# Optimization experiments

Measured on AMD Instinct MI355X. Metric: run time of the kernel, lower is better.

Reference implementation:

```python
import jax, jax.numpy as jnp
from jax import lax
import numpy as np

B, W, M, F = 8, 20, 512, 16
H = 128          # n_hidden
HALF = 64        # half_hid
K = 10           # conv out channels
LONG_K = W // 2  # dilated conv kernel


def setup_inputs() -> dict:
    key = jax.random.key(0)
    ks = jax.random.split(key, 24)
    s = 0.1  # weight scale (xavier-ish)
    return {
        "X": jax.random.normal(ks[0], (B, W, M, F), jnp.float32),
        "Y": jax.random.uniform(ks[1], (B, M), jnp.float32),
        "adj": jax.random.uniform(ks[2], (M, M), jnp.float32),
        "V": jax.random.normal(ks[3], (HALF,), jnp.float32) * s,
        "bv": jax.random.normal(ks[4], (1,), jnp.float32) * s,
        "W1": jax.random.normal(ks[5], (HALF, H), jnp.float32) * s,
        "b1": jax.random.normal(ks[6], (HALF,), jnp.float32) * s,
        "W2": jax.random.normal(ks[7], (HALF, H), jnp.float32) * s,
        "Wb": jax.random.normal(ks[8], (M, M), jnp.float32) * s,
        "wb": jax.random.normal(ks[9], (1,), jnp.float32) * s,
        "conv_w": jax.random.normal(ks[10], (K, F, W), jnp.float32) * s,
        "conv_b": jax.random.normal(ks[11], (K,), jnp.float32) * s,
        "convl_w": jax.random.normal(ks[12], (K, F, LONG_K), jnp.float32) * s,
        "convl_b": jax.random.normal(ks[13], (K,), jnp.float32) * s,
        "gru_Wih": jax.random.normal(ks[14], (3 * H, F), jnp.float32) * s,
        "gru_Whh": jax.random.normal(ks[15], (3 * H, H), jnp.float32) * s,
        "gru_bih": jax.random.normal(ks[16], (3 * H,), jnp.float32) * s,
        "gru_bhh": jax.random.normal(ks[17], (3 * H,), jnp.float32) * s,
        "gc1_W": jax.random.normal(ks[18], (3 * K, H), jnp.float32) * s,
        "gc1_b": jax.random.normal(ks[19], (H,), jnp.float32) * s,
        "gc2_W": jax.random.normal(ks[20], (H, K), jnp.float32) * s,
        "gc2_b": jax.random.normal(ks[21], (K,), jnp.float32) * s,
        "out_W": jax.random.normal(ks[22], (1, H + K), jnp.float32) * s,
        "out_b": jax.random.normal(ks[23], (1,), jnp.float32) * s,
    }


def _gru_last(xseq, Wih, Whh, bih, bhh):
    # xseq: (N, T, F) -> last hidden (N, H), PyTorch GRU gate order r,z,n
    n_hid = Whh.shape[1]
    def step(h, x_t):
        gx = x_t @ Wih.T + bih
        gh = h @ Whh.T + bhh
        xr, xz, xn = jnp.split(gx, 3, axis=-1)
        hr, hz, hn = jnp.split(gh, 3, axis=-1)
        r = jax.nn.sigmoid(xr + hr)
        z = jax.nn.sigmoid(xz + hz)
        n = jnp.tanh(xn + r * hn)
        return (1.0 - z) * n + z * h, None
    h0 = jnp.zeros((xseq.shape[0], n_hid), xseq.dtype)
    hT, _ = lax.scan(step, h0, jnp.moveaxis(xseq, 1, 0))
    return hT


def _forward(X, Y, adj, V, bv, W1, b1, W2, Wb, wb, conv_w, conv_b, convl_w,
             convl_b, gru_Wih, gru_Whh, gru_bih, gru_bhh, gc1_W, gc1_b,
             gc2_W, gc2_b, out_W, out_b):
    b, w, m, f = X.shape
    # ---- temporal branch: GRU per node ----
    x = jnp.transpose(X, (0, 2, 1, 3)).reshape(b * m, w, f)
    last_hid = _gru_last(x, gru_Wih, gru_Whh, gru_bih, gru_bhh).reshape(b, m, -1)
    out_temporal = last_hid
    # ---- attention-style adaptive adjacency ----
    # hid_rpt_m[b,i,j]=last_hid[b,j]; hid_rpt_w[b,i,j]=last_hid[b,i]
    p1 = jnp.einsum('bjh,kh->bjk', last_hid, W1)  # pairs with column index j
    p2 = jnp.einsum('bih,kh->bik', last_hid, W2)  # pairs with row index i
    pre = p1[:, None, :, :] + p2[:, :, None, :] + b1  # (b,m,m,half)
    a_mx = jnp.einsum('bijk,k->bij', jax.nn.elu(pre), V) + bv[0]
    # F.normalize(p=2, dim=1)
    nrm = jnp.sqrt(jnp.sum(a_mx * a_mx, axis=1, keepdims=True))
    a_mx = a_mx / jnp.maximum(nrm, 1e-12)
    # ---- per-node conv1d (vectorized over nodes) ----
    Xc = jnp.transpose(X, (0, 2, 3, 1)).reshape(b * m, f, w)  # (bm, f, w)
    dn = ('NCH', 'OIH', 'NCH')
    r = lax.conv_general_dilated(Xc, conv_w, (1,), 'VALID', dimension_numbers=dn)
    r = r + conv_b[None, :, None]                      # (bm, K, 1)
    rl = lax.conv_general_dilated(Xc, convl_w, (1,), 'VALID',
                                  rhs_dilation=(2,), dimension_numbers=dn)
    rl = rl + convl_b[None, :, None]                   # (bm, K, long_out)
    r_cat = jnp.concatenate([r, rl], axis=-1)          # (bm, K, 1+long_out)
    r_l = jax.nn.relu(r_cat.reshape(b, m, -1))         # (b, m, (1+long_out)*K)
    # ---- gate learned adjacency with fixed adjacency ----
    c = jax.nn.sigmoid(jnp.einsum('bij,jk->bik', a_mx, Wb) + wb[0])
    A = adj[None] * c + a_mx * (1.0 - c)               # (b,m,m)
    # ---- graph convolutions: out = A @ (x @ W) + b ----
    h1 = jax.nn.relu(jnp.einsum('bij,bjh->bih', A, r_l @ gc1_W) + gc1_b)
    out_spatial = jax.nn.relu(jnp.einsum('bij,bjh->bih', A, h1 @ gc2_W) + gc2_b)
    # ---- readout ----
    out = jnp.concatenate([out_spatial, out_temporal], axis=-1)
    out = (out @ out_W.T + out_b).squeeze(-1)          # (b, m)
    y = out.reshape(-1)
    Yf = Y.reshape(-1)
    # BCE with logits: softplus(y) - Y*y, averaged
    loss = jnp.mean(jax.nn.softplus(y) - Yf * y)
    return loss, jax.nn.sigmoid(y)


def reference(X, Y, adj, V, bv, W1, b1, W2, Wb, wb, conv_w, conv_b, convl_w,
              convl_b, gru_Wih, gru_Whh, gru_bih, gru_bhh, gc1_W, gc1_b,
              gc2_W, gc2_b, out_W, out_b):
    return _forward(X, Y, adj, V, bv, W1, b1, W2, Wb, wb, conv_w, conv_b,
                    convl_w, convl_b, gru_Wih, gru_Whh, gru_bih, gru_bhh,
                    gc1_W, gc1_b, gc2_W, gc2_b, out_W, out_b)
```

## Files before the change

### kernel.cpp

```cpp
#include <hip/hip_runtime.h>
#include <math.h>

#define Bn 8
#define Wn 20
#define Mn 512
#define Fn 16
#define Hn 128
#define HALFn 64
#define Kn 10

typedef __attribute__((ext_vector_type(8))) short short8;
typedef __attribute__((ext_vector_type(4))) float f32x4;
typedef unsigned short ushort_t;

__device__ __forceinline__ float sigmoidf_(float x) {
  return 1.0f / (1.0f + __expf(-x));
}
__device__ __forceinline__ float tanhf_(float x) {
  float xx = fminf(fmaxf(x, -15.f), 15.f);
  float e = __expf(2.f * xx);
  return (e - 1.f) / (e + 1.f);
}
__device__ __forceinline__ float reluf_(float x) { return fmaxf(x, 0.f); }
__device__ __forceinline__ float eluf_(float x) {
  return (x > 0.f) ? x : (__expf(x) - 1.f);
}
__device__ __forceinline__ ushort_t bf16_rne(float v) {
  unsigned u = __float_as_uint(v);
  u += 0x7FFFu + ((u >> 16) & 1u);
  return (ushort_t)(u >> 16);
}
__device__ __forceinline__ float bf16_to_f(ushort_t b) {
  return __uint_as_float(((unsigned)b) << 16);
}

__global__ __launch_bounds__(256) void pack_kernel(
    const float* __restrict__ Whh, const float* __restrict__ Wih,
    const float* __restrict__ Wb, ushort_t* __restrict__ Bpack,
    ushort_t* __restrict__ WbT_hi, ushort_t* __restrict__ WbT_lo,
    float* __restrict__ ssq, float* __restrict__ d_out) {
  int tid = threadIdx.x;
  if (blockIdx.x < 240) {
    int idx = blockIdx.x * 256 + tid;
    if (idx < 4096) ssq[idx] = 0.f;
    if (idx == 0) d_out[0] = 0.f;
    if (idx >= 24 * 5 * 512) return;
    int j = idx & 7;
    int lane = (idx >> 3) & 63;
    int ks = (idx >> 9) % 5;
    int nt = idx / (5 * 512);
    int k = ks * 32 + (lane >> 4) * 8 + j;
    int g = (nt & 7) * 16 + (nt >> 3) * 128 + (lane & 15);
    float val = 0.f;
    if (k < 128) val = Whh[g * 128 + k];
    else if (k < 144) val = Wih[g * 16 + (k - 128)];
    ushort_t hb = bf16_rne(val);
    float lo = val - bf16_to_f(hb);
    Bpack[(((long)nt * 5 + ks) * 2 + 0) * 512 + lane * 8 + j] = hb;
    Bpack[(((long)nt * 5 + ks) * 2 + 1) * 512 + lane * 8 + j] = bf16_rne(lo);
  } else {
    int t = blockIdx.x - 240;
    int k0 = (t >> 3) * 64, j0 = (t & 7) * 64;
    __shared__ float wt[64][65];
    for (int idx = tid; idx < 4096; idx += 256) {
      int r = idx >> 6, c = idx & 63;
      wt[r][c] = Wb[(long)(k0 + r) * 512 + j0 + c];
    }
    __syncthreads();
    for (int idx = tid; idx < 4096; idx += 256) {
      int r = idx >> 6, c = idx & 63;
      float v = wt[c][r];
      ushort_t hb = bf16_rne(v);
      WbT_hi[(long)(j0 + r) * 512 + k0 + c] = hb;
      WbT_lo[(long)(j0 + r) * 512 + k0 + c] = bf16_rne(v - bf16_to_f(hb));
    }
  }
}

#define LDK 168
__global__ __launch_bounds__(512, 2) void gru_kernel(
    const float* __restrict__ X, const ushort_t* __restrict__ Bpack,
    const float* __restrict__ bih, const float* __restrict__ bhh,
    const float* __restrict__ W1, const float* __restrict__ W2,
    const float* __restrict__ b1, float* __restrict__ last_hid,
    float* __restrict__ p1, float* __restrict__ p2) {
  const int tid = threadIdx.x;
  const int wave = tid >> 6;
  const int lane = tid & 63;
  const int quad = lane >> 4;
  const int jl = lane & 15;
  const int j0 = wave * 16;
  const int blk = blockIdx.x;
  const int b = blk >> 5;
  const int m0 = (blk & 31) * 16;

  __shared__ __align__(16) ushort_t smem_hs[2 * 16 * LDK];
  ushort_t* h_hi = smem_hs;
  ushort_t* h_lo = smem_hs + 16 * LDK;

  short8 frR[5][2], frZ[5][2], frN[4][2], frXN[2];
#pragma unroll
  for (int ks = 0; ks < 5; ++ks) {
#pragma unroll
    for (int p = 0; p < 2; ++p) {
      frR[ks][p] = *(const short8*)&Bpack[(((long)(wave) * 5 + ks) * 2 + p) * 512 + lane * 8];
      frZ[ks][p] = *(const short8*)&Bpack[(((long)(8 + wave) * 5 + ks) * 2 + p) * 512 + lane * 8];
    }
  }
#pragma unroll
  for (int ks = 0; ks < 4; ++ks) {
#pragma unroll
    for (int p = 0; p < 2; ++p)
      frN[ks][p] = *(const short8*)&Bpack[(((long)(16 + wave) * 5 + ks) * 2 + p) * 512 + lane * 8];
  }
#pragma unroll
  for (int p = 0; p < 2; ++p)
    frXN[p] = *(const short8*)&Bpack[(((long)(16 + wave) * 5 + 4) * 2 + p) * 512 + lane * 8];

  const float cr  = bih[j0 + jl] + bhh[j0 + jl];
  const float cz  = bih[128 + j0 + jl] + bhh[128 + j0 + jl];
  const float cnx = bih[256 + j0 + jl];
  const float cnh = bhh[256 + j0 + jl];

  for (int i = tid; i < 16 * LDK; i += 512) { h_hi[i] = 0; h_lo[i] = 0; }

  const float* Xb = X + (long)b * (Wn * Mn * Fn) + (long)m0 * Fn;
  float x0 = 0.f;
  if (tid < 256) x0 = Xb[tid];
  __syncthreads();
  if (tid < 256) {
    int s = tid >> 4, f = tid & 15;
    ushort_t hb = bf16_rne(x0);
    h_hi[s * LDK + 128 + f] = hb;
    h_lo[s * LDK + 128 + f] = bf16_rne(x0 - bf16_to_f(hb));
  }
  __syncthreads();

  float hp[4] = {0.f, 0.f, 0.f, 0.f};

  for (int t = 0; t < Wn; ++t) {
    float xpre = 0.f;
    {
      int tt = (t < Wn - 1) ? (t + 1) : (Wn - 1);
      if (tid < 256) xpre = Xb[(long)tt * (Mn * Fn) + tid];
    }
    f32x4 aR = {0.f, 0.f, 0.f, 0.f}, aZ = {0.f, 0.f, 0.f, 0.f};
    f32x4 aHN = {0.f, 0.f, 0.f, 0.f}, aXN = {0.f, 0.f, 0.f, 0.f};
#pragma unroll
    for (int ks = 0; ks < 5; ++ks) {
      short8 ah = *(const short8*)&h_hi[jl * LDK + ks * 32 + quad * 8];
      short8 al = *(const short8*)&h_lo[jl * LDK + ks * 32 + quad * 8];
      aR = __builtin_amdgcn_mfma_f32_16x16x32_bf16(ah, frR[ks][0], aR, 0, 0, 0);
      aR = __builtin_amdgcn_mfma_f32_16x16x32_bf16(ah, frR[ks][1], aR, 0, 0, 0);
      aR = __builtin_amdgcn_mfma_f32_16x16x32_bf16(al, frR[ks][0], aR, 0, 0, 0);
      aZ = __builtin_amdgcn_mfma_f32_16x16x32_bf16(ah, frZ[ks][0], aZ, 0, 0, 0);
      aZ = __builtin_amdgcn_mfma_f32_16x16x32_bf16(ah, frZ[ks][1], aZ, 0, 0, 0);
      aZ = __builtin_amdgcn_mfma_f32_16x16x32_bf16(al, frZ[ks][0], aZ, 0, 0, 0);
      if (ks < 4) {
        aHN = __builtin_amdgcn_mfma_f32_16x16x32_bf16(ah, frN[ks][0], aHN, 0, 0, 0);
        aHN = __builtin_amdgcn_mfma_f32_16x16x32_bf16(ah, frN[ks][1], aHN, 0, 0, 0);
        aHN = __builtin_amdgcn_mfma_f32_16x16x32_bf16(al, frN[ks][0], aHN, 0, 0, 0);
      } else {
        aXN = __builtin_amdgcn_mfma_f32_16x16x32_bf16(ah, frXN[0], aXN, 0, 0, 0);
        aXN = __builtin_amdgcn_mfma_f32_16x16x32_bf16(ah, frXN[1], aXN, 0, 0, 0);
        aXN = __builtin_amdgcn_mfma_f32_16x16x32_bf16(al, frXN[0], aXN, 0, 0, 0);
      }
    }
    __syncthreads();
#pragma unroll
    for (int reg = 0; reg < 4; ++reg) {
      float r = sigmoidf_(aR[reg] + cr);
      float z = sigmoidf_(aZ[reg] + cz);
      float n = tanhf_(aXN[reg] + cnx + r * (aHN[reg] + cnh));
      float h = (1.f - z) * n + z * hp[reg];
      hp[reg] = h;
      int s = quad * 4 + reg;
      ushort_t hb = bf16_rne(h);
      h_hi[s * LDK + j0 + jl] = hb;
      h_lo[s * LDK + j0 + jl] = bf16_rne(h - bf16_to_f(hb));
    }
    if (tid < 256 && t < Wn - 1) {
      int s = tid >> 4, f = tid & 15;
      ushort_t hb = bf16_rne(xpre);
      h_hi[s * LDK + 128 + f] = hb;
      h_lo[s * LDK + 128 + f] = bf16_rne(xpre - bf16_to_f(hb));
    }
    __syncthreads();
  }

  float* hs_f = (float*)smem_hs;
#pragma unroll
  for (int reg = 0; reg < 4; ++reg) {
    int s = quad * 4 + reg;
    float h = hp[reg];
    last_hid[(long)(blk * 16 + s) * Hn + j0 + jl] = h;
    hs_f[s * 132 + j0 + jl] = h;
  }
  __syncthreads();
  {
    int k = tid & 63;
    int part = (tid >> 6) & 1;
    int sg = tid >> 7;
    const float* Wp = part ? W2 : W1;
    float a[4];
    float init = part ? 0.f : b1[k];
    a[0] = a[1] = a[2] = a[3] = init;
    for (int h = 0; h < 128; h += 4) {
      float4 w = *(const float4*)&Wp[k * 128 + h];
#pragma unroll
      for (int rr = 0; rr < 4; ++rr) {
        float4 q = *(const float4*)&hs_f[(sg * 4 + rr) * 132 + h];
        a[rr] += q.x * w.x + q.y * w.y + q.z * w.z + q.w * w.w;
      }
    }
    float* outp = part ? p2 : p1;
#pragma unroll
    for (int rr = 0; rr < 4; ++rr)
      outp[(long)(blk * 16 + sg * 4 + rr) * 64 + k] = a[rr];
  }
}

__global__ __launch_bounds__(128) void conv_t1_kernel(
    const float* __restrict__ X, const float* __restrict__ conv_w,
    const float* __restrict__ conv_b, const float* __restrict__ convl_w,
    const float* __restrict__ convl_b, const float* __restrict__ gc1_W,
    ushort_t* __restrict__ t1T_hi, ushort_t* __restrict__ t1T_lo) {
  int tid = threadIdx.x;
  int n0 = blockIdx.x * 8;
  int b = n0 >> 9, m0 = n0 & 511;
  __shared__ float xs[8][16][20];
  __shared__ float cw[3200];
  __shared__ float clw[1600];
  __shared__ float rs[8][32];
  for (int idx = tid; idx < 3200; idx += 128) cw[idx] = conv_w[idx];
  for (int idx = tid; idx < 1600; idx += 128) clw[idx] = convl_w[idx];
  for (int w = 0; w < 20; ++w)
    xs[tid >> 4][tid & 15][w] = X[((long)(b * 20 + w) * 512 + m0) * 16 + tid];
  __syncthreads();
  if (tid < 80) {
    int s = tid / 10, k = tid % 10;
    float a0 = conv_b[k];
    float l0 = convl_b[k], l1 = convl_b[k];
    for (int f = 0; f < 16; ++f) {
#pragma unroll
      for (int w = 0; w < 20; ++w) a0 = fmaf(xs[s][f][w], cw[k * 320 + f * 20 + w], a0);
#pragma unroll
      for (int q = 0; q < 10; ++q) {
        float wv = clw[k * 160 + f * 10 + q];
        l0 = fmaf(xs[s][f][2 * q], wv, l0);
        l1 = fmaf(xs[s][f][2 * q + 1], wv, l1);
      }
    }
    rs[s][k * 3 + 0] = reluf_(a0);
    rs[s][k * 3 + 1] = reluf_(l0);
    rs[s][k * 3 + 2] = reluf_(l1);
  }
  __syncthreads();
  float w[30];
#pragma unroll
  for (int q = 0; q < 30; ++q) w[q] = gc1_W[q * 128 + tid];
  long base = ((long)b * 128 + tid) * 512 + m0;
#pragma unroll
  for (int s = 0; s < 8; ++s) {
    float a = 0.f;
#pragma unroll
    for (int q = 0; q < 30; ++q) a = fmaf(rs[s][q], w[q], a);
    ushort_t hb = bf16_rne(a);
    t1T_hi[base + s] = hb;
    t1T_lo[base + s] = bf16_rne(a - bf16_to_f(hb));
  }
}

__global__ __launch_bounds__(256) void amx_kernel(
    const float* __restrict__ p1, const float* __restrict__ p2,
    const float* __restrict__ V, const float* __restrict__ bv,
    float* __restrict__ amx, float* __restrict__ ssq) {
  int tid = threadIdx.x;
  int j0 = blockIdx.x * 32, i0 = blockIdx.y * 32, bz = blockIdx.z;
  __shared__ float p1s[32][68];
  __shared__ float p2s[32][68];
  __shared__ float Vs[64];
  __shared__ float cred[16][33];
  if (tid < 64) Vs[tid] = V[tid];
  {
    int rr = tid >> 3, c0 = (tid & 7) * 8;
    *(float4*)&p1s[rr][c0]     = *(const float4*)&p1[(long)(bz * 512 + j0 + rr) * 64 + c0];
    *(float4*)&p1s[rr][c0 + 4] = *(const float4*)&p1[(long)(bz * 512 + j0 + rr) * 64 + c0 + 4];
    *(float4*)&p2s[rr][c0]     = *(const float4*)&p2[(long)(bz * 512 + i0 + rr) * 64 + c0];
    *(float4*)&p2s[rr][c0 + 4] = *(const float4*)&p2[(long)(bz * 512 + i0 + rr) * 64 + c0 + 4];
  }
  __syncthreads();
  int r0 = tid >> 4, c0 = tid & 15;
  float acc[2][2] = {{0.f, 0.f}, {0.f, 0.f}};
  for (int k = 0; k < 64; ++k) {
    float vj0 = p1s[c0][k], vj1 = p1s[c0 + 16][k];
    float vi0 = p2s[r0][k], vi1 = p2s[r0 + 16][k];
    float vk = Vs[k];
    acc[0][0] = fmaf(eluf_(vj0 + vi0), vk, acc[0][0]);
    acc[0][1] = fmaf(eluf_(vj1 + vi0), vk, acc[0][1]);
    acc[1][0] = fmaf(eluf_(vj0 + vi1), vk, acc[1][0]);
    acc[1][1] = fmaf(eluf_(vj1 + vi1), vk, acc[1][1]);
  }
  float bvv = bv[0];
  float s2[2] = {0.f, 0.f};
#pragma unroll
  for (int a = 0; a < 2; ++a)
#pragma unroll
    for (int c = 0; c < 2; ++c) {
      float v = acc[a][c] + bvv;
      amx[((long)(bz * 512 + i0 + r0 + a * 16)) * 512 + j0 + c0 + c * 16] = v;
      s2[c] += v * v;
    }
  cred[r0][c0] = s2[0];
  cred[r0][c0 + 16] = s2[1];
  __syncthreads();
  if (tid < 32) {
    float s = 0.f;
#pragma unroll
    for (int p = 0; p < 16; ++p) s += cred[p][tid];
    atomicAdd(&ssq[bz * 512 + j0 + tid], s);
  }
}

#define CPK 40
__global__ __launch_bounds__(128, 2) void gemm_cA(
    const float* __restrict__ amx, const ushort_t* __restrict__ WbT_hi,
    const ushort_t* __restrict__ WbT_lo, const float* __restrict__ adj,
    const float* __restrict__ wb, const float* __restrict__ ssq,
    float* __restrict__ A) {
  const int bz = blockIdx.z;
  const int i0 = blockIdx.y * 128;
  const int j0 = blockIdx.x * 64;
  const int tid = threadIdx.x;
  const int wave = tid >> 6;
  const int lane = tid & 63;
  const int quad = lane >> 4, jl = lane & 15;

  __shared__ __align__(16) ushort_t Ahi[128][CPK];
  __shared__ __align__(16) ushort_t Alo[128][CPK];
  __shared__ __align__(16) ushort_t Bhi[64][CPK];
  __shared__ __align__(16) ushort_t Blo[64][CPK];
  __shared__ float rs_s[512];

  const float* Abase = amx + (long)bz * 262144;
  const float* sb = ssq + bz * 512;
  for (int i = tid; i < 512; i += 128)
    rs_s[i] = 1.f / fmaxf(sqrtf(sb[i]), 1e-12f);

  f32x4 acc[4][4];
#pragma unroll
  for (int a = 0; a < 4; ++a)
#pragma unroll
    for (int c = 0; c < 4; ++c) acc[a][c] = (f32x4){0.f, 0.f, 0.f, 0.f};

  for (int kk0 = 0; kk0 < 512; kk0 += 32) {
    __syncthreads();
#pragma unroll
    for (int l = 0; l < 8; ++l) {
      int e = l * 512 + tid * 4;
      int r = e >> 5, kq = e & 31;
      float4 v = *(const float4*)&Abase[(long)(i0 + r) * 512 + kk0 + kq];
      float4 sc = *(const float4*)&rs_s[kk0 + kq];
      float vv[4] = {v.x * sc.x, v.y * sc.y, v.z * sc.z, v.w * sc.w};
#pragma unroll
      for (int q = 0; q < 4; ++q) {
        ushort_t hb = bf16_rne(vv[q]);
        Ahi[r][kq + q] = hb;
        Alo[r][kq + q] = bf16_rne(vv[q] - bf16_to_f(hb));
      }
    }
#pragma unroll
    for (int l = 0; l < 2; ++l) {
      int e = l * 1024 + tid * 8;
      int r = e >> 5, kc = e & 31;
      *(uint4*)&Bhi[r][kc] = *(const uint4*)&WbT_hi[(long)(j0 + r) * 512 + kk0 + kc];
      *(uint4*)&Blo[r][kc] = *(const uint4*)&WbT_lo[(long)(j0 + r) * 512 + kk0 + kc];
    }
    __syncthreads();
    short8 ah[4], al[4], bh[4], bl[4];
#pragma unroll
    for (int tm = 0; tm < 4; ++tm) {
      ah[tm] = *(const short8*)&Ahi[wave * 64 + tm * 16 + jl][quad * 8];
      al[tm] = *(const short8*)&Alo[wave * 64 + tm * 16 + jl][quad * 8];
    }
#pragma unroll
    for (int tn = 0; tn < 4; ++tn) {
      bh[tn] = *(const short8*)&Bhi[tn * 16 + jl][quad * 8];
      bl[tn] = *(const short8*)&Blo[tn * 16 + jl][quad * 8];
    }
#pragma unroll
    for (int tm = 0; tm < 4; ++tm)
#pragma unroll
      for (int tn = 0; tn < 4; ++tn) {
        acc[tm][tn] = __builtin_amdgcn_mfma_f32_16x16x32_bf16(ah[tm], bh[tn], acc[tm][tn], 0, 0, 0);
        acc[tm][tn] = __builtin_amdgcn_mfma_f32_16x16x32_bf16(ah[tm], bl[tn], acc[tm][tn], 0, 0, 0);
        acc[tm][tn] = __builtin_amdgcn_mfma_f32_16x16x32_bf16(al[tm], bh[tn], acc[tm][tn], 0, 0, 0);
      }
  }

  const float wbv = wb[0];
#pragma unroll
  for (int tn = 0; tn < 4; ++tn) {
    int j = j0 + tn * 16 + jl;
    float sj = rs_s[j];
#pragma unroll
    for (int tm = 0; tm < 4; ++tm) {
#pragma unroll
      for (int reg = 0; reg < 4; ++reg) {
        int i = i0 + wave * 64 + tm * 16 + quad * 4 + reg;
        long ofs = (long)bz * 262144 + (long)i * 512 + j;
        float c = sigmoidf_(acc[tm][tn][reg] + wbv);
        float am = Abase[(long)i * 512 + j] * sj;
        float ad = adj[(long)i * 512 + j];
        A[ofs] = ad * c + am * (1.f - c);
      }
    }
  }
}

__global__ __launch_bounds__(256, 2) void gemm_h1t2(
    const float* __restrict__ A, const ushort_t* __restrict__ t1T_hi,
    const ushort_t* __restrict__ t1T_lo, const float* __restrict__ gc1_b,
    const float* __restrict__ gc2_W, float* __restrict__ t2) {
  const int bz = blockIdx.y;
  const int i0 = blockIdx.x * 32;
  const int tid = threadIdx.x;
  const int wave = tid >> 6;
  const int lane = tid & 63;
  const int quad = lane >> 4, jl = lane & 15;

  __shared__ __align__(16) ushort_t Ahi[32][CPK];
  __shared__ __align__(16) ushort_t Alo[32][CPK];
  __shared__ __align__(16) ushort_t Bhi[128][CPK];
  __shared__ __align__(16) ushort_t Blo[128][CPK];
  __shared__ float h1s[32][132];
  __shared__ float gw[1280];

  const float* Ab = A + (long)bz * 262144;
  for (int idx = tid; idx < 1280; idx += 256) gw[idx] = gc2_W[idx];

  f32x4 acc[2][2];
#pragma unroll
  for (int a = 0; a < 2; ++a)
#pragma unroll
    for (int c = 0; c < 2; ++c) acc[a][c] = (f32x4){0.f, 0.f, 0.f, 0.f};

  for (int kk0 = 0; kk0 < 512; kk0 += 32) {
    __syncthreads();
    {
      int e = tid * 4;
      int r = e >> 5, kq = e & 31;
      float4 v = *(const float4*)&Ab[(long)(i0 + r) * 512 + kk0 + kq];
      float vv[4] = {v.x, v.y, v.z, v.w};
#pragma unroll
      for (int q = 0; q < 4; ++q) {
        ushort_t hb = bf16_rne(vv[q]);
        Ahi[r][kq + q] = hb;
        Alo[r][kq + q] = bf16_rne(vv[q] - bf16_to_f(hb));
      }
    }
#pragma unroll
    for (int l = 0; l < 2; ++l) {
      int e = l * 2048 + tid * 8;
      int r = e >> 5, kc = e & 31;
      *(uint4*)&Bhi[r][kc] = *(const uint4*)&t1T_hi[((long)bz * 128 + r) * 512 + kk0 + kc];
      *(uint4*)&Blo[r][kc] = *(const uint4*)&t1T_lo[((long)bz * 128 + r) * 512 + kk0 + kc];
    }
    __syncthreads();
    short8 ah[2], al[2], bh[2], bl[2];
#pragma unroll
    for (int tm = 0; tm < 2; ++tm) {
      ah[tm] = *(const short8*)&Ahi[tm * 16 + jl][quad * 8];
      al[tm] = *(const short8*)&Alo[tm * 16 + jl][quad * 8];
    }
#pragma unroll
    for (int tn = 0; tn < 2; ++tn) {
      bh[tn] = *(const short8*)&Bhi[wave * 32 + tn * 16 + jl][quad * 8];
      bl[tn] = *(const short8*)&Blo[wave * 32 + tn * 16 + jl][quad * 8];
    }
#pragma unroll
    for (int tm = 0; tm < 2; ++tm)
#pragma unroll
      for (int tn = 0; tn < 2; ++tn) {
        acc[tm][tn] = __builtin_amdgcn_mfma_f32_16x16x32_bf16(ah[tm], bh[tn], acc[tm][tn], 0, 0, 0);
        acc[tm][tn] = __builtin_amdgcn_mfma_f32_16x16x32_bf16(ah[tm], bl[tn], acc[tm][tn], 0, 0, 0);
        acc[tm][tn] = __builtin_amdgcn_mfma_f32_16x16x32_bf16(al[tm], bh[tn], acc[tm][tn], 0, 0, 0);
      }
  }
  __syncthreads();
#pragma unroll
  for (int tm = 0; tm < 2; ++tm)
#pragma unroll
    for (int tn = 0; tn < 2; ++tn) {
      int n = wave * 32 + tn * 16 + jl;
      float bb = gc1_b[n];
#pragma unroll
      for (int reg = 0; reg < 4; ++reg) {
        int r = tm * 16 + quad * 4 + reg;
        h1s[r][n] = reluf_(acc[tm][tn][reg] + bb);
      }
    }
  __syncthreads();
  for (int e = tid; e < 320; e += 256) {
    int r = e / 10, c = e % 10;
    float a = 0.f;
#pragma unroll 4
    for (int k = 0; k < 128; ++k) a = fmaf(h1s[r][k], gw[k * 10 + c], a);
    t2[((long)bz * 512 + i0 + r) * 10 + c] = a;
  }
}

__global__ __launch_bounds__(256) void spat_readout(
    const float* __restrict__ A, const float* __restrict__ t2,
    const float* __restrict__ gc2_b, const float* __restrict__ last_hid,
    const float* __restrict__ out_W, const float* __restrict__ out_b,
    const float* __restrict__ Y, float* __restrict__ d_out) {
  int tid = threadIdx.x;
  int bz = blockIdx.y;
  int i0 = blockIdx.x * 16;
  __shared__ float t2s[5120];
  __shared__ float wS[138];
  __shared__ float osps[16][12];
  for (int idx = tid; idx < 5120; idx += 256) t2s[idx] = t2[(long)bz * 5120 + idx];
  for (int idx = tid; idx < 138; idx += 256) wS[idx] = out_W[idx];
  __syncthreads();
  int r = tid >> 4, sk = tid & 15;
  const float* Arow = A + (long)bz * 262144 + (long)(i0 + r) * 512;
  float acc[10] = {0, 0, 0, 0, 0, 0, 0, 0, 0, 0};
  for (int k = sk; k < 512; k += 16) {
    float av = Arow[k];
    const float* tp = &t2s[k * 10];
#pragma unroll
    for (int c = 0; c < 10; ++c) acc[c] = fmaf(av, tp[c], acc[c]);
  }
#pragma unroll
  for (int off = 8; off; off >>= 1)
#pragma unroll
    for (int c = 0; c < 10; ++c) acc[c] += __shfl_xor(acc[c], off);
  if (sk == 0) {
#pragma unroll
    for (int c = 0; c < 10; ++c) osps[r][c] = reluf_(acc[c] + gc2_b[c]);
  }
  __syncthreads();
  float l = 0.f;
  if (tid < 16) {
    int gid = bz * 512 + i0 + tid;
    float y = out_b[0];
#pragma unroll
    for (int k = 0; k < 10; ++k) y = fmaf(osps[tid][k], wS[k], y);
    const float* hp = &last_hid[(long)gid * 128];
    for (int h = 0; h < 128; h += 4) {
      float4 hv = *(const float4*)&hp[h];
      y = fmaf(hv.x, wS[10 + h + 0], y);
      y = fmaf(hv.y, wS[10 + h + 1], y);
      y = fmaf(hv.z, wS[10 + h + 2], y);
      y = fmaf(hv.w, wS[10 + h + 3], y);
    }
    d_out[1 + gid] = sigmoidf_(y);
    l = fmaxf(y, 0.f) + log1pf(__expf(-fabsf(y))) - Y[gid] * y;
  }
  if (tid < 64) {
#pragma unroll
    for (int off = 8; off; off >>= 1) l += __shfl_down(l, off);
    if (tid == 0) atomicAdd(d_out, l * (1.0f / 4096.f));
  }
}

extern "C" void kernel_launch(void* const* d_in, const int* in_sizes, int n_in,
                              void* d_out, int out_size, void* d_ws, size_t ws_size,
                              hipStream_t stream) {
  const float* X       = (const float*)d_in[0];
  const float* Y       = (const float*)d_in[1];
  const float* adj     = (const float*)d_in[2];
  const float* V       = (const float*)d_in[3];
  const float* bv      = (const float*)d_in[4];
  const float* W1      = (const float*)d_in[5];
  const float* b1      = (const float*)d_in[6];
  const float* W2      = (const float*)d_in[7];
  const float* Wb      = (const float*)d_in[8];
  const float* wb      = (const float*)d_in[9];
  const float* conv_w  = (const float*)d_in[10];
  const float* conv_b  = (const float*)d_in[11];
  const float* convl_w = (const float*)d_in[12];
  const float* convl_b = (const float*)d_in[13];
  const float* gWih    = (const float*)d_in[14];
  const float* gWhh    = (const float*)d_in[15];
  const float* gbih    = (const float*)d_in[16];
  const float* gbhh    = (const float*)d_in[17];
  const float* gc1_W   = (const float*)d_in[18];
  const float* gc1_b   = (const float*)d_in[19];
  const float* gc2_W   = (const float*)d_in[20];
  const float* gc2_b   = (const float*)d_in[21];
  const float* out_W   = (const float*)d_in[22];
  const float* out_b   = (const float*)d_in[23];
  float* out = (float*)d_out;

  float* ws = (float*)d_ws;
  float* lhid  = ws; ws += 524288;
  float* p1    = ws; ws += 262144;
  float* p2    = ws; ws += 262144;
  float* amx   = ws; ws += 2097152;
  float* ssq   = ws; ws += 4096;
  float* Abuf  = ws; ws += 2097152;
  float* t2    = ws; ws += 40960;
  float* Bpkf  = ws; ws += 122880;
  float* WbTf  = ws; ws += 262144;
  float* t1Tf  = ws; ws += 524288;
  if (ws_size < (size_t)(ws - (float*)d_ws) * sizeof(float)) return;
  ushort_t* Bpack  = (ushort_t*)Bpkf;
  ushort_t* WbT_hi = (ushort_t*)WbTf;
  ushort_t* WbT_lo = WbT_hi + 262144;
  ushort_t* t1T_hi = (ushort_t*)t1Tf;
  ushort_t* t1T_lo = t1T_hi + 524288;

  pack_kernel<<<304, 256, 0, stream>>>(gWhh, gWih, Wb, Bpack, WbT_hi, WbT_lo,
                                       ssq, out);
  gru_kernel<<<256, 512, 0, stream>>>(X, Bpack, gbih, gbhh, W1, W2, b1,
                                      lhid, p1, p2);
  conv_t1_kernel<<<512, 128, 0, stream>>>(X, conv_w, conv_b, convl_w, convl_b,
                                          gc1_W, t1T_hi, t1T_lo);
  amx_kernel<<<dim3(16, 16, 8), 256, 0, stream>>>(p1, p2, V, bv, amx, ssq);
  gemm_cA<<<dim3(8, 4, 8), 128, 0, stream>>>(amx, WbT_hi, WbT_lo, adj, wb,
                                             ssq, Abuf);
  gemm_h1t2<<<dim3(16, 8), 256, 0, stream>>>(Abuf, t1T_hi, t1T_lo, gc1_b,
                                             gc2_W, t2);
  spat_readout<<<dim3(32, 8), 256, 0, stream>>>(Abuf, t2, gc2_b, lhid,
                                                out_W, out_b, Y, out);
}
```

Measured before the change: 268.4 us.

## Double-buffer GRU hidden state, split MFMA accumulators, halve h1t2 row tile

The GRU recurrence now ping-pongs the bf16 hi/lo hidden-state buffers in shared memory, which drops one of the two block-wide barriers per timestep. It also splits the R/Z/HN accumulators into two chains by k-step parity to shorten the dependent MFMA chain. Separately, gemm_h1t2 processes 16 rows per block instead of 32 and launches twice as many blocks to spread the small GEMM across more CUs. The cost is double the GRU LDS footprint and reloading the B tile in twice as many blocks.

New measurement: 263.2 us. No clear change (-1.9%).

```diff
diff --git a/kernel.cpp b/kernel.cpp
--- a/kernel.cpp
+++ b/kernel.cpp
@@ -78,6 +78,7 @@
 }
 
 #define LDK 168
+#define HSZ (16 * LDK)
 __global__ __launch_bounds__(512, 2) void gru_kernel(
     const float* __restrict__ X, const ushort_t* __restrict__ Bpack,
     const float* __restrict__ bih, const float* __restrict__ bhh,
@@ -94,9 +95,7 @@
   const int b = blk >> 5;
   const int m0 = (blk & 31) * 16;
 
-  __shared__ __align__(16) ushort_t smem_hs[2 * 16 * LDK];
-  ushort_t* h_hi = smem_hs;
-  ushort_t* h_lo = smem_hs + 16 * LDK;
+  __shared__ __align__(16) ushort_t smem_hs[4 * HSZ];
 
   short8 frR[5][2], frZ[5][2], frN[4][2], frXN[2];
 #pragma unroll
@@ -122,7 +121,7 @@
   const float cnx = bih[256 + j0 + jl];
   const float cnh = bhh[256 + j0 + jl];
 
-  for (int i = tid; i < 16 * LDK; i += 512) { h_hi[i] = 0; h_lo[i] = 0; }
+  for (int i = tid; i < 4 * HSZ; i += 512) smem_hs[i] = 0;
 
   const float* Xb = X + (long)b * (Wn * Mn * Fn) + (long)m0 * Fn;
   float x0 = 0.f;
@@ -131,59 +130,61 @@
   if (tid < 256) {
     int s = tid >> 4, f = tid & 15;
     ushort_t hb = bf16_rne(x0);
-    h_hi[s * LDK + 128 + f] = hb;
-    h_lo[s * LDK + 128 + f] = bf16_rne(x0 - bf16_to_f(hb));
+    smem_hs[0 * HSZ + s * LDK + 128 + f] = hb;
+    smem_hs[2 * HSZ + s * LDK + 128 + f] = bf16_rne(x0 - bf16_to_f(hb));
   }
   __syncthreads();
 
   float hp[4] = {0.f, 0.f, 0.f, 0.f};
 
   for (int t = 0; t < Wn; ++t) {
+    const int cur = t & 1, nxt = cur ^ 1;
+    const int hiC = cur * HSZ, loC = (2 + cur) * HSZ;
+    const int hiN = nxt * HSZ, loN = (2 + nxt) * HSZ;
     float xpre = 0.f;
-    {
-      int tt = (t < Wn - 1) ? (t + 1) : (Wn - 1);
-      if (tid < 256) xpre = Xb[(long)tt * (Mn * Fn) + tid];
-    }
-    f32x4 aR = {0.f, 0.f, 0.f, 0.f}, aZ = {0.f, 0.f, 0.f, 0.f};
-    f32x4 aHN = {0.f, 0.f, 0.f, 0.f}, aXN = {0.f, 0.f, 0.f, 0.f};
+    if (tid < 256 && t < Wn - 1) xpre = Xb[(long)(t + 1) * (Mn * Fn) + tid];
+
+    f32x4 aR[2], aZ[2], aHN[2], aXN;
+    aR[0] = aR[1] = aZ[0] = aZ[1] = aHN[0] = aHN[1] = aXN = (f32x4){0.f, 0.f, 0.f, 0.f};
 #pragma unroll
     for (int ks = 0; ks < 5; ++ks) {
-      short8 ah = *(const short8*)&h_hi[jl * LDK + ks * 32 + quad * 8];
-      short8 al = *(const short8*)&h_lo[jl * LDK + ks * 32 + quad * 8];
-      aR = __builtin_amdgcn_mfma_f32_16x16x32_bf16(ah, frR[ks][0], aR, 0, 0, 0);
-      aR = __builtin_amdgcn_mfma_f32_16x16x32_bf16(ah, frR[ks][1], aR, 0, 0, 0);
-      aR = __builtin_amdgcn_mfma_f32_16x16x32_bf16(al, frR[ks][0], aR, 0, 0, 0);
-      aZ = __builtin_amdgcn_mfma_f32_16x16x32_bf16(ah, frZ[ks][0], aZ, 0, 0, 0);
-      aZ = __builtin_amdgcn_mfma_f32_16x16x32_bf16(ah, frZ[ks][1], aZ, 0, 0, 0);
-      aZ = __builtin_amdgcn_mfma_f32_16x16x32_bf16(al, frZ[ks][0], aZ, 0, 0, 0);
+      const int p = ks & 1;
+      short8 ah = *(const short8*)&smem_hs[hiC + jl * LDK + ks * 32 + quad * 8];
+      short8 al = *(const short8*)&smem_hs[loC + jl * LDK + ks * 32 + quad * 8];
+      aR[p] = __builtin_amdgcn_mfma_f32_16x16x32_bf16(ah, frR[ks][0], aR[p], 0, 0, 0);
+      aR[p] = __builtin_amdgcn_mfma_f32_16x16x32_bf16(ah, frR[ks][1], aR[p], 0, 0, 0);
+      aR[p] = __builtin_amdgcn_mfma_f32_16x16x32_bf16(al, frR[ks][0], aR[p], 0, 0, 0);
+      aZ[p] = __builtin_amdgcn_mfma_f32_16x16x32_bf16(ah, frZ[ks][0], aZ[p], 0, 0, 0);
+      aZ[p] = __builtin_amdgcn_mfma_f32_16x16x32_bf16(ah, frZ[ks][1], aZ[p], 0, 0, 0);
+      aZ[p] = __builtin_amdgcn_mfma_f32_16x16x32_bf16(al, frZ[ks][0], aZ[p], 0, 0, 0);
       if (ks < 4) {
-        aHN = __builtin_amdgcn_mfma_f32_16x16x32_bf16(ah, frN[ks][0], aHN, 0, 0, 0);
-        aHN = __builtin_amdgcn_mfma_f32_16x16x32_bf16(ah, frN[ks][1], aHN, 0, 0, 0);
-        aHN = __builtin_amdgcn_mfma_f32_16x16x32_bf16(al, frN[ks][0], aHN, 0, 0, 0);
+        aHN[p] = __builtin_amdgcn_mfma_f32_16x16x32_bf16(ah, frN[ks][0], aHN[p], 0, 0, 0);
+        aHN[p] = __builtin_amdgcn_mfma_f32_16x16x32_bf16(ah, frN[ks][1], aHN[p], 0, 0, 0);
+        aHN[p] = __builtin_amdgcn_mfma_f32_16x16x32_bf16(al, frN[ks][0], aHN[p], 0, 0, 0);
       } else {
         aXN = __builtin_amdgcn_mfma_f32_16x16x32_bf16(ah, frXN[0], aXN, 0, 0, 0);
         aXN = __builtin_amdgcn_mfma_f32_16x16x32_bf16(ah, frXN[1], aXN, 0, 0, 0);
         aXN = __builtin_amdgcn_mfma_f32_16x16x32_bf16(al, frXN[0], aXN, 0, 0, 0);
       }
     }
-    __syncthreads();
+
 #pragma unroll
     for (int reg = 0; reg < 4; ++reg) {
-      float r = sigmoidf_(aR[reg] + cr);
-      float z = sigmoidf_(aZ[reg] + cz);
-      float n = tanhf_(aXN[reg] + cnx + r * (aHN[reg] + cnh));
+      float r = sigmoidf_(aR[0][reg] + aR[1][reg] + cr);
+      float z = sigmoidf_(aZ[0][reg] + aZ[1][reg] + cz);
+      float n = tanhf_(aXN[reg] + cnx + r * (aHN[0][reg] + aHN[1][reg] + cnh));
       float h = (1.f - z) * n + z * hp[reg];
       hp[reg] = h;
       int s = quad * 4 + reg;
       ushort_t hb = bf16_rne(h);
-      h_hi[s * LDK + j0 + jl] = hb;
-      h_lo[s * LDK + j0 + jl] = bf16_rne(h - bf16_to_f(hb));
+      smem_hs[hiN + s * LDK + j0 + jl] = hb;
+      smem_hs[loN + s * LDK + j0 + jl] = bf16_rne(h - bf16_to_f(hb));
     }
     if (tid < 256 && t < Wn - 1) {
       int s = tid >> 4, f = tid & 15;
       ushort_t hb = bf16_rne(xpre);
-      h_hi[s * LDK + 128 + f] = hb;
-      h_lo[s * LDK + 128 + f] = bf16_rne(xpre - bf16_to_f(hb));
+      smem_hs[hiN + s * LDK + 128 + f] = hb;
+      smem_hs[loN + s * LDK + 128 + f] = bf16_rne(xpre - bf16_to_f(hb));
     }
     __syncthreads();
   }
@@ -423,41 +424,37 @@
     const ushort_t* __restrict__ t1T_lo, const float* __restrict__ gc1_b,
     const float* __restrict__ gc2_W, float* __restrict__ t2) {
   const int bz = blockIdx.y;
-  const int i0 = blockIdx.x * 32;
+  const int i0 = blockIdx.x * 16;
   const int tid = threadIdx.x;
   const int wave = tid >> 6;
   const int lane = tid & 63;
   const int quad = lane >> 4, jl = lane & 15;
 
-  __shared__ __align__(16) ushort_t Ahi[32][CPK];
-  __shared__ __align__(16) ushort_t Alo[32][CPK];
+  __shared__ __align__(16) ushort_t Ahi[16][CPK];
+  __shared__ __align__(16) ushort_t Alo[16][CPK];
   __shared__ __align__(16) ushort_t Bhi[128][CPK];
   __shared__ __align__(16) ushort_t Blo[128][CPK];
-  __shared__ float h1s[32][132];
+  __shared__ float h1s[16][132];
   __shared__ float gw[1280];
 
   const float* Ab = A + (long)bz * 262144;
   for (int idx = tid; idx < 1280; idx += 256) gw[idx] = gc2_W[idx];
 
-  f32x4 acc[2][2];
-#pragma unroll
-  for (int a = 0; a < 2; ++a)
-#pragma unroll
-    for (int c = 0; c < 2; ++c) acc[a][c] = (f32x4){0.f, 0.f, 0.f, 0.f};
+  f32x4 acc[2];
+  acc[0] = acc[1] = (f32x4){0.f, 0.f, 0.f, 0.f};
 
   for (int kk0 = 0; kk0 < 512; kk0 += 32) {
     __syncthreads();
     {
-      int e = tid * 4;
+      int e = tid * 2;
       int r = e >> 5, kq = e & 31;
-      float4 v = *(const float4*)&Ab[(long)(i0 + r) * 512 + kk0 + kq];
-      float vv[4] = {v.x, v.y, v.z, v.w};
-#pragma unroll
-      for (int q = 0; q < 4; ++q) {
-        ushort_t hb = bf16_rne(vv[q]);
-        Ahi[r][kq + q] = hb;
-        Alo[r][kq + q] = bf16_rne(vv[q] - bf16_to_f(hb));
-      }
+      float2 v = *(const float2*)&Ab[(long)(i0 + r) * 512 + kk0 + kq];
+      ushort_t hb0 = bf16_rne(v.x);
+      Ahi[r][kq] = hb0;
+      Alo[r][kq] = bf16_rne(v.x - bf16_to_f(hb0));
+      ushort_t hb1 = bf16_rne(v.y);
+      Ahi[r][kq + 1] = hb1;
+      Alo[r][kq + 1] = bf16_rne(v.y - bf16_to_f(hb1));
     }
 #pragma unroll
     for (int l = 0; l < 2; ++l) {
@@ -467,42 +464,35 @@
       *(uint4*)&Blo[r][kc] = *(const uint4*)&t1T_lo[((long)bz * 128 + r) * 512 + kk0 + kc];
     }
     __syncthreads();
-    short8 ah[2], al[2], bh[2], bl[2];
-#pragma unroll
-    for (int tm = 0; tm < 2; ++tm) {
-      ah[tm] = *(const short8*)&Ahi[tm * 16 + jl][quad * 8];
-      al[tm] = *(const short8*)&Alo[tm * 16 + jl][quad * 8];
-    }
+    short8 ah = *(const short8*)&Ahi[jl][quad * 8];
+    short8 al = *(const short8*)&Alo[jl][quad * 8];
+    short8 bh[2], bl[2];
 #pragma unroll
     for (int tn = 0; tn < 2; ++tn) {
       bh[tn] = *(const short8*)&Bhi[wave * 32 + tn * 16 + jl][quad * 8];
       bl[tn] = *(const short8*)&Blo[wave * 32 + tn * 16 + jl][quad * 8];
     }
 #pragma unroll
-    for (int tm = 0; tm < 2; ++tm)
-#pragma unroll
-      for (int tn = 0; tn < 2; ++tn) {
-        acc[tm][tn] = __builtin_amdgcn_mfma_f32_16x16x32_bf16(ah[tm], bh[tn], acc[tm][tn], 0, 0, 0);
-        acc[tm][tn] = __builtin_amdgcn_mfma_f32_16x16x32_bf16(ah[tm], bl[tn], acc[tm][tn], 0, 0, 0);
-        acc[tm][tn] = __builtin_amdgcn_mfma_f32_16x16x32_bf16(al[tm], bh[tn], acc[tm][tn], 0, 0, 0);
-      }
-  }
-  __syncthreads();
-#pragma unroll
-  for (int tm = 0; tm < 2; ++tm)
-#pragma unroll
     for (int tn = 0; tn < 2; ++tn) {
-      int n = wave * 32 + tn * 16 + jl;
-      float bb = gc1_b[n];
-#pragma unroll
-      for (int reg = 0; reg < 4; ++reg) {
-        int r = tm * 16 + quad * 4 + reg;
-        h1s[r][n] = reluf_(acc[tm][tn][reg] + bb);
-      }
-    }
-  __syncthreads();
-  for (int e = tid; e < 320; e += 256) {
-    int r = e / 10, c = e % 10;
+      acc[tn] = __builtin_amdgcn_mfma_f32_16x16x32_bf16(ah, bh[tn], acc[tn], 0, 0, 0);
+      acc[tn] = __builtin_amdgcn_mfma_f32_16x16x32_bf16(ah, bl[tn], acc[tn], 0, 0, 0);
+      acc[tn] = __builtin_amdgcn_mfma_f32_16x16x32_bf16(al, bh[tn], acc[tn], 0, 0, 0);
+    }
+  }
+  __syncthreads();
+#pragma unroll
+  for (int tn = 0; tn < 2; ++tn) {
+    int n = wave * 32 + tn * 16 + jl;
+    float bb = gc1_b[n];
+#pragma unroll
+    for (int reg = 0; reg < 4; ++reg) {
+      int r = quad * 4 + reg;
+      h1s[r][n] = reluf_(acc[tn][reg] + bb);
+    }
+  }
+  __syncthreads();
+  if (tid < 160) {
+    int r = tid / 10, c = tid % 10;
     float a = 0.f;
 #pragma unroll 4
     for (int k = 0; k < 128; ++k) a = fmaf(h1s[r][k], gw[k * 10 + c], a);
@@ -622,7 +612,7 @@
   amx_kernel<<<dim3(16, 16, 8), 256, 0, stream>>>(p1, p2, V, bv, amx, ssq);
   gemm_cA<<<dim3(8, 4, 8), 128, 0, stream>>>(amx, WbT_hi, WbT_lo, adj, wb,
                                              ssq, Abuf);
-  gemm_h1t2<<<dim3(16, 8), 256, 0, stream>>>(Abuf, t1T_hi, t1T_lo, gc1_b,
+  gemm_h1t2<<<dim3(32, 8), 256, 0, stream>>>(Abuf, t1T_hi, t1T_lo, gc1_b,
                                              gc2_W, t2);
   spat_readout<<<dim3(32, 8), 256, 0, stream>>>(Abuf, t2, gc2_b, lhid,
                                                 out_W, out_b, Y, out);
```
